# Optimization experiments

Hardware: AMD Instinct MI355X
Metric: run time of the kernel (lower is better)

The kernel has to match this reference:

```python
import jax, jax.numpy as jnp
import numpy as np

N_ENT = 100000   # n_entities
N_REL = 64       # n_relations
E_DIM = 64       # e_dim == r_dim (rel2ent is None)
K = 32           # neighbors per entity
B = 1024         # batch of seed entities
SLOPE = 0.2      # LeakyReLU negative_slope


def _xavier(key, shape, fan_in, fan_out):
    b = (6.0 / (fan_in + fan_out)) ** 0.5
    return jax.random.uniform(key, shape, jnp.float32, -b, b)


def setup_inputs() -> dict:
    key = jax.random.key(0)
    ks = jax.random.split(key, 10)
    E = _xavier(ks[0], (N_ENT, E_DIM), N_ENT, E_DIM)          # entity_embs.weight
    R = _xavier(ks[1], (N_REL, E_DIM), N_REL, E_DIM)          # relation_embs.weight
    att_w1 = _xavier(ks[2], (E_DIM, 2 * E_DIM), 2 * E_DIM, E_DIM)  # attention[0], no bias
    att_w2 = _xavier(ks[3], (E_DIM, E_DIM), E_DIM, E_DIM)          # attention[2], no bias
    att_w3 = _xavier(ks[4], (1, E_DIM), E_DIM, 1)                  # attention[4], no bias
    wx_w = _xavier(ks[5], (E_DIM, E_DIM), E_DIM, E_DIM)            # Wx[0].weight
    wx_b = jnp.zeros((E_DIM,), jnp.float32)                        # Wx[0].bias
    wc_w = _xavier(ks[6], (E_DIM, 2 * E_DIM), 2 * E_DIM, E_DIM)    # W_concat.weight
    wc_b = jnp.zeros((E_DIM,), jnp.float32)                        # W_concat.bias
    entity_idx = jax.random.randint(ks[7], (B,), 0, N_ENT)
    adj_entity = jax.random.randint(ks[8], (N_ENT, K), 0, N_ENT)
    adj_relation = jax.random.randint(ks[9], (N_ENT, K), 0, N_REL)
    return {
        "entity_idx": entity_idx, "adj_entity": adj_entity, "adj_relation": adj_relation,
        "E": E, "R": R, "att_w1": att_w1, "att_w2": att_w2, "att_w3": att_w3,
        "wx_w": wx_w, "wx_b": wx_b, "wc_w": wc_w, "wc_b": wc_b,
    }


def _lookup(W, idx):
    # nn.Embedding(max_norm=1): rows whose L2 norm exceeds 1 are renormalized.
    e = W[idx]
    n = jnp.linalg.norm(e, axis=-1, keepdims=True)
    return e * jnp.where(n > 1.0, 1.0 / (n + 1e-7), 1.0)


def _forward(entity_idx, adj_entity, adj_relation, E, R,
             att_w1, att_w2, att_w3, wx_w, wx_b, wc_w, wc_b):
    leaky = lambda x: jnp.where(x >= 0, x, SLOPE * x)
    # attention MLP on cat([h, r]): split first linear so the broadcast h term
    # is computed once per batch row instead of materializing [B, N, 2e].
    w1h, w1r = att_w1[:, :E_DIM], att_w1[:, E_DIM:]

    def gat(h, r, t):
        # h: [B, e] (broadcast over neighbors), r,t: [B, N, e]
        hid = jax.nn.relu(jnp.einsum('be,fe->bf', h, w1h)[:, None, :]
                          + jnp.einsum('bne,fe->bnf', r, w1r))
        hid = jax.nn.relu(jnp.einsum('bnf,gf->bng', hid, att_w2))
        a = jax.nn.sigmoid(jnp.einsum('bng,og->bno', hid, att_w3)[..., 0])  # [B, N]
        w = jax.nn.softmax(a, axis=-1)
        agg = jnp.einsum('bn,bne->be', w, t)       # softmax-weighted neighbor sum
        return agg @ wx_w.T + wx_b                 # per-head Linear (n_heads=1)

    Bsz = entity_idx.shape[0]
    # hop-1 / hop-2 neighbor index gathers (get_neighbors)
    ent1 = adj_entity[entity_idx]                  # [B, K]
    rel1 = adj_relation[entity_idx]                # [B, K]
    ent2 = adj_entity[ent1].reshape(Bsz, -1)       # [B, K*K]
    rel2 = adj_relation[ent1].reshape(Bsz, -1)     # [B, K*K]

    h = _lookup(E, entity_idx)                     # [B, e]
    t1 = _lookup(E, ent1)                          # [B, K, e]
    t2 = _lookup(E, ent2)                          # [B, K*K, e]
    r1 = _lookup(R, rel1)
    r2 = _lookup(R, rel2)

    # iter 0: seed entity broadcast as head
    v1 = leaky(gat(h, r1, t1))                                      # [B, e]
    emb1 = leaky(jnp.concatenate([h, v1], -1) @ wc_w.T + wc_b)      # aggregate 'concat'
    # iter 1: summed hop-1 neighborhood as head
    hsum = t1.sum(axis=1)                                           # [B, e]
    v2 = leaky(gat(hsum, r2, t2))
    emb2 = leaky(jnp.concatenate([hsum, v2], -1) @ wc_w.T + wc_b)
    # sum_aggregator 'concat': e_u = cat(embs[2], cat(embs[1], embs[0]))
    return jnp.concatenate([emb2, emb1, h], axis=-1)                # [B, 3e]


def reference(entity_idx, adj_entity, adj_relation, E, R,
              att_w1, att_w2, att_w3, wx_w, wx_b, wc_w, wc_b):
    return _forward(entity_idx, adj_entity, adj_relation, E, R,
                    att_w1, att_w2, att_w3, wx_w, wx_b, wc_w, wc_b)
```

## Files before the change

kernel.cpp:

```cpp
#include <hip/hip_runtime.h>

#define SLOPE 0.2f

__device__ __forceinline__ float leaky(float x) { return x >= 0.f ? x : SLOPE * x; }

enum : int {
  OFF_PT   = 0,
  OFF_W2T  = OFF_PT + 4096,
  OFF_A3   = OFF_W2T + 4096,
  OFF_WXT  = OFF_A3 + 64,
  OFF_WXB  = OFF_WXT + 4096,
  OFF_WCT  = OFF_WXB + 64,
  OFF_WCB  = OFF_WCT + 8192,
  OFF_W1HT = OFF_WCB + 64,
  WS_FLOATS = OFF_W1HT + 4096,
  EBF_U32  = 3200000
};

__global__ __launch_bounds__(256) void k1_prep(
    const float* __restrict__ R, const float* __restrict__ w1,
    const float* __restrict__ w2, const float* __restrict__ w3,
    const float* __restrict__ wxw, const float* __restrict__ wxb,
    const float* __restrict__ wcw, const float* __restrict__ wcb,
    const float* __restrict__ E, float* __restrict__ ws) {
  int tid = threadIdx.x;
  if (blockIdx.x >= 8) {
    const float4* E4 = (const float4*)E;
    unsigned long long* Ebf2 =
        (unsigned long long*)((unsigned*)ws + WS_FLOATS);
    int nvec = EBF_U32 / 2;
    int stride = (gridDim.x - 8) * 256;
    for (int i = (blockIdx.x - 8) * 256 + tid; i < nvec; i += stride) {
      float4 f = E4[i];
      unsigned ua = __float_as_uint(f.x); ua += 0x7FFFu + ((ua >> 16) & 1u);
      unsigned ub = __float_as_uint(f.y); ub += 0x7FFFu + ((ub >> 16) & 1u);
      unsigned uc = __float_as_uint(f.z); uc += 0x7FFFu + ((uc >> 16) & 1u);
      unsigned ud = __float_as_uint(f.w); ud += 0x7FFFu + ((ud >> 16) & 1u);
      unsigned lo = (ua >> 16) | (ub & 0xFFFF0000u);
      unsigned hi = (uc >> 16) | (ud & 0xFFFF0000u);
      unsigned long long o = (unsigned long long)lo |
                             ((unsigned long long)hi << 32);
      __builtin_nontemporal_store(o, &Ebf2[i]);
    }
    return;
  }
  __shared__ float Rn[64 * 65];
  int wv = tid >> 6, lane = tid & 63;
  for (int r = wv; r < 64; r += 4) {
    float v = R[r * 64 + lane];
    float ss = v * v;
    #pragma unroll
    for (int m = 1; m < 64; m <<= 1) ss += __shfl_xor(ss, m, 64);
    float n = sqrtf(ss);
    float sc = n > 1.f ? 1.f / (n + 1e-7f) : 1.f;
    Rn[r * 65 + lane] = v * sc;
  }
  __syncthreads();
  int gt = blockIdx.x * 256 + tid;
  for (int i = gt; i < 4096; i += 2048) {
    int f = i >> 6, r = i & 63;
    float acc = 0.f;
    #pragma unroll
    for (int e = 0; e < 64; ++e) acc += Rn[r * 65 + e] * w1[f * 128 + 64 + e];
    ws[OFF_PT + f * 64 + r] = acc;
  }
  for (int i = gt; i < 4096; i += 2048) {
    int f = i >> 6, g = i & 63;
    ws[OFF_W2T + i] = w2[g * 64 + f];
  }
  for (int i = gt; i < 4096; i += 2048) {
    int e = i >> 6, f = i & 63;
    ws[OFF_WXT + i]  = wxw[f * 64 + e];
    ws[OFF_W1HT + i] = w1[f * 128 + e];
  }
  for (int i = gt; i < 8192; i += 2048) {
    int e = i >> 6, f = i & 63;
    ws[OFF_WCT + i] = wcw[f * 128 + e];
  }
  if (gt < 64) {
    ws[OFF_A3 + gt]  = w3[gt];
    ws[OFF_WXB + gt] = wxb[gt];
    ws[OFF_WCB + gt] = wcb[gt];
  }
}

__global__ __launch_bounds__(256) void k_main(
    const int* __restrict__ entity_idx, const int* __restrict__ adj_entity,
    const int* __restrict__ adj_relation, const float* __restrict__ E,
    const float* __restrict__ ws, float* __restrict__ out) {
  __shared__ float s_t1[32 * 64];
  __shared__ float s_partA[4][64], s_partB[4][64];
  __shared__ int   s_ent1[32], s_rel1[32];
  __shared__ unsigned s_ei[1024];
  __shared__ float s_w[1024];
  __shared__ float s_h[64], s_hs[64], s_hq1[64], s_hq2[64];
  __shared__ float s_at1[64], s_at2[64], s_agg1[64], s_agg2[64], s_v1[64], s_v2[64];
  __shared__ float s_L1, s_L2;
  int b = blockIdx.x, tid = threadIdx.x, wv = tid >> 6, lane = tid & 63;
  int idx = entity_idx[b];

  if (tid < 64) s_h[tid] = E[(long)idx * 64 + tid];
  if (tid >= 64 && tid < 96) {
    int i = tid - 64;
    s_ent1[i] = adj_entity[(long)idx * 32 + i];
    s_rel1[i] = adj_relation[(long)idx * 32 + i];
  }
  if (tid == 0) s_L2 = 0.f;
  __syncthreads();

  #pragma unroll
  for (int i = 0; i < 4; ++i) {
    int n = tid + i * 256;
    int j = n >> 5, i2 = n & 31;
    long base = (long)s_ent1[j] * 32 + i2;
    unsigned ei = (unsigned)adj_entity[base];
    unsigned ri = (unsigned)adj_relation[base];
    s_ei[n] = ei | (ri << 24);
  }
  {
    float hs = 0.f;
    #pragma unroll
    for (int k = 0; k < 8; ++k) {
      int n = wv * 8 + k;
      float v = E[(long)s_ent1[n] * 64 + lane];
      s_t1[n * 64 + lane] = v;
      hs += v;
    }
    s_partA[wv][lane] = hs;
  }
  __syncthreads();
  if (tid < 64)
    s_hs[tid] = s_partA[0][tid] + s_partA[1][tid] + s_partA[2][tid] + s_partA[3][tid];
  __syncthreads();

  {
    const float* src = (wv < 2) ? s_h : s_hs;
    int e0 = (wv & 1) * 32;
    float p = 0.f;
    #pragma unroll 8
    for (int e = 0; e < 32; ++e) p += ws[OFF_W1HT + (e0 + e) * 64 + lane] * src[e0 + e];
    s_partB[wv][lane] = p;
  }
  __syncthreads();
  if (tid < 64) s_hq1[tid] = s_partB[0][tid] + s_partB[1][tid];
  else if (tid < 128) { int i = tid - 64; s_hq2[i] = s_partB[2][i] + s_partB[3][i]; }
  __syncthreads();

  {
    int swv = __builtin_amdgcn_readfirstlane(wv);
    const float* W2T = ws + OFF_W2T;
    const float* A3  = ws + OFF_A3;
    const float* PT  = ws + OFF_PT;
    float acc2[16];
    #pragma unroll
    for (int i = 0; i < 16; ++i) acc2[i] = 0.f;
    int g0 = swv * 16;
    #pragma unroll 2
    for (int f = 0; f < 64; ++f) {
      float ptv = PT[f * 64 + lane];
      float h2 = fmaxf(s_hq2[f] + ptv, 0.f);
      const float* w = W2T + f * 64 + g0;
      #pragma unroll
      for (int i = 0; i < 16; ++i) acc2[i] += w[i] * h2;
    }
    float s2 = 0.f;
    #pragma unroll
    for (int i = 0; i < 16; ++i) s2 += A3[g0 + i] * fmaxf(acc2[i], 0.f);
    s_partB[wv][lane] = s2;
  }
  __syncthreads();
  if (tid < 64) {
    float t = s_partB[0][tid] + s_partB[1][tid] + s_partB[2][tid] + s_partB[3][tid];
    float a = 1.f / (1.f + __expf(-t));
    s_at2[tid] = __expf(a);
  }
  __syncthreads();

  {
    float wsum = 0.f;
    #pragma unroll
    for (int i = 0; i < 4; ++i) {
      int n = tid + i * 256;
      float wgt = s_at2[s_ei[n] >> 24];
      s_w[n] = wgt;
      wsum += wgt;
    }
    #pragma unroll
    for (int m = 1; m < 64; m <<= 1) wsum += __shfl_xor(wsum, m, 64);
    if (lane == 0) atomicAdd(&s_L2, wsum);
  }
  __syncthreads();

  {
    const uint4* Ebf = (const uint4*)((const unsigned*)ws + WS_FLOATS);
    int sub8 = lane >> 3, eg8 = lane & 7;
    int rbase = wv * 8 + sub8;
    int swv = __builtin_amdgcn_readfirstlane(wv);
    const float* W2T = ws + OFF_W2T;
    const float* A3  = ws + OFF_A3;
    const float* PT  = ws + OFF_PT;
    int g0 = swv * 16;
    float acc[8], acc1[16];
    #pragma unroll
    for (int k = 0; k < 8; ++k) acc[k] = 0.f;
    #pragma unroll
    for (int i = 0; i < 16; ++i) acc1[i] = 0.f;

    #pragma unroll 1
    for (int t = 0; t < 8; ++t) {
      uint4 v[4];
      float wgt[4];
      #pragma unroll
      for (int j = 0; j < 4; ++j) {
        int n = (t * 4 + j) * 32 + rbase;
        v[j] = Ebf[(long)(s_ei[n] & 0xFFFFFFu) * 8 + eg8];
        wgt[j] = s_w[n];
      }
      #pragma unroll
      for (int ff = 0; ff < 8; ++ff) {
        int f = t * 8 + ff;
        float ptv = PT[f * 64 + lane];
        float h1 = fmaxf(s_hq1[f] + ptv, 0.f);
        const float* w = W2T + f * 64 + g0;
        #pragma unroll
        for (int i = 0; i < 16; ++i) acc1[i] += w[i] * h1;
      }
      #pragma unroll
      for (int j = 0; j < 4; ++j) {
        float w = wgt[j];
        acc[0] += w * __uint_as_float(v[j].x << 16);
        acc[1] += w * __uint_as_float(v[j].x & 0xFFFF0000u);
        acc[2] += w * __uint_as_float(v[j].y << 16);
        acc[3] += w * __uint_as_float(v[j].y & 0xFFFF0000u);
        acc[4] += w * __uint_as_float(v[j].z << 16);
        acc[5] += w * __uint_as_float(v[j].z & 0xFFFF0000u);
        acc[6] += w * __uint_as_float(v[j].w << 16);
        acc[7] += w * __uint_as_float(v[j].w & 0xFFFF0000u);
      }
    }
    float s1 = 0.f;
    #pragma unroll
    for (int i = 0; i < 16; ++i) s1 += A3[g0 + i] * fmaxf(acc1[i], 0.f);
    s_partA[wv][lane] = s1;
    #pragma unroll
    for (int m = 8; m < 64; m <<= 1) {
      #pragma unroll
      for (int k = 0; k < 8; ++k) acc[k] += __shfl_xor(acc[k], m, 64);
    }
    if (sub8 == 0) {
      #pragma unroll
      for (int k = 0; k < 8; ++k) s_partB[wv][eg8 * 8 + k] = acc[k];
    }
  }
  __syncthreads();
  if (tid < 64) {
    float t = s_partA[0][tid] + s_partA[1][tid] + s_partA[2][tid] + s_partA[3][tid];
    float a = 1.f / (1.f + __expf(-t));
    s_at1[tid] = __expf(a);
  } else if (tid < 128) {
    int i = tid - 64;
    float a = s_partB[0][i] + s_partB[1][i] + s_partB[2][i] + s_partB[3][i];
    s_agg2[i] = a / s_L2;
  }
  __syncthreads();

  if (tid < 32) {
    float w = s_at1[s_rel1[tid]];
    #pragma unroll
    for (int m = 1; m < 32; m <<= 1) w += __shfl_xor(w, m, 64);
    if (tid == 0) s_L1 = w;
  }
  {
    float a1 = 0.f;
    #pragma unroll
    for (int k = 0; k < 8; ++k) {
      int n = wv * 8 + k;
      a1 += s_at1[s_rel1[n]] * s_t1[n * 64 + lane];
    }
    s_partA[wv][lane] = a1;
  }
  __syncthreads();
  if (tid < 64) {
    float a = s_partA[0][tid] + s_partA[1][tid] + s_partA[2][tid] + s_partA[3][tid];
    s_agg1[tid] = a / s_L1;
  }
  __syncthreads();

  {
    const float* src = (wv < 2) ? s_agg1 : s_agg2;
    int e0 = (wv & 1) * 32;
    float p = 0.f;
    #pragma unroll 8
    for (int e = 0; e < 32; ++e)
      p += ws[OFF_WXT + (e0 + e) * 64 + lane] * src[e0 + e];
    s_partA[wv][lane] = p;
  }
  __syncthreads();
  if (tid < 64) {
    s_v1[tid] = leaky(ws[OFF_WXB + tid] + s_partA[0][tid] + s_partA[1][tid]);
  } else if (tid < 128) {
    int i = tid - 64;
    s_v2[i] = leaky(ws[OFF_WXB + i] + s_partA[2][i] + s_partA[3][i]);
  }
  __syncthreads();

  {
    const float* src = (wv == 0) ? s_h : (wv == 1) ? s_v1 : (wv == 2) ? s_hs : s_v2;
    int e0 = (wv & 1) * 64;
    float p = 0.f;
    #pragma unroll 8
    for (int e = 0; e < 64; ++e)
      p += ws[OFF_WCT + (e0 + e) * 64 + lane] * src[e];
    s_partB[wv][lane] = p;
  }
  __syncthreads();
  if (tid < 64) {
    float o = ws[OFF_WCB + tid] + s_partB[0][tid] + s_partB[1][tid];
    out[b * 192 + 64 + tid]  = leaky(o);
    out[b * 192 + 128 + tid] = s_h[tid];
  } else if (tid < 128) {
    int i = tid - 64;
    float o = ws[OFF_WCB + i] + s_partB[2][i] + s_partB[3][i];
    out[b * 192 + i] = leaky(o);
  }
}

extern "C" void kernel_launch(void* const* d_in, const int* in_sizes, int n_in,
                              void* d_out, int out_size, void* d_ws, size_t ws_size,
                              hipStream_t stream) {
  const int* entity_idx   = (const int*)d_in[0];
  const int* adj_entity   = (const int*)d_in[1];
  const int* adj_relation = (const int*)d_in[2];
  const float* E          = (const float*)d_in[3];
  const float* R          = (const float*)d_in[4];
  const float* att_w1     = (const float*)d_in[5];
  const float* att_w2     = (const float*)d_in[6];
  const float* att_w3     = (const float*)d_in[7];
  const float* wx_w       = (const float*)d_in[8];
  const float* wx_b       = (const float*)d_in[9];
  const float* wc_w       = (const float*)d_in[10];
  const float* wc_b       = (const float*)d_in[11];
  float* out              = (float*)d_out;
  float* ws               = (float*)d_ws;

  hipLaunchKernelGGL(k1_prep, dim3(1608), dim3(256), 0, stream,
                     R, att_w1, att_w2, att_w3, wx_w, wx_b, wc_w, wc_b, E, ws);
  hipLaunchKernelGGL(k_main, dim3(1024), dim3(256), 0, stream,
                     entity_idx, adj_entity, adj_relation, E, ws, out);
}
```

Baseline: 149.5 us.

## Double k_main block to 512 threads and split per-block work across eight waves

Raises the main kernel from 4 to 8 wavefronts per block. Every stage (hop-2 gather, attention MLP slices, reductions, final linears) is repartitioned so each wave does half as much work, with partial sums reduced over 8 slots. The aim is more latency hiding for the random bf16 gathers and shorter per-wave serial chains. The cost is more partial-sum reduction work, and each block keeps its extra barriers.

```diff
diff --git a/kernel.cpp b/kernel.cpp
--- a/kernel.cpp
+++ b/kernel.cpp
@@ -84,12 +84,12 @@
   }
 }
 
-__global__ __launch_bounds__(256) void k_main(
+__global__ __launch_bounds__(512, 8) void k_main(
     const int* __restrict__ entity_idx, const int* __restrict__ adj_entity,
     const int* __restrict__ adj_relation, const float* __restrict__ E,
     const float* __restrict__ ws, float* __restrict__ out) {
   __shared__ float s_t1[32 * 64];
-  __shared__ float s_partA[4][64], s_partB[4][64];
+  __shared__ float s_partA[8][64], s_partB[8][64];
   __shared__ int   s_ent1[32], s_rel1[32];
   __shared__ unsigned s_ei[1024];
   __shared__ float s_w[1024];
@@ -109,8 +109,8 @@
   __syncthreads();
 
   #pragma unroll
-  for (int i = 0; i < 4; ++i) {
-    int n = tid + i * 256;
+  for (int i = 0; i < 2; ++i) {
+    int n = tid + i * 512;
     int j = n >> 5, i2 = n & 31;
     long base = (long)s_ent1[j] * 32 + i2;
     unsigned ei = (unsigned)adj_entity[base];
@@ -120,8 +120,8 @@
   {
     float hs = 0.f;
     #pragma unroll
-    for (int k = 0; k < 8; ++k) {
-      int n = wv * 8 + k;
+    for (int k = 0; k < 4; ++k) {
+      int n = wv * 4 + k;
       float v = E[(long)s_ent1[n] * 64 + lane];
       s_t1[n * 64 + lane] = v;
       hs += v;
@@ -129,21 +129,29 @@
     s_partA[wv][lane] = hs;
   }
   __syncthreads();
-  if (tid < 64)
-    s_hs[tid] = s_partA[0][tid] + s_partA[1][tid] + s_partA[2][tid] + s_partA[3][tid];
-  __syncthreads();
-
-  {
-    const float* src = (wv < 2) ? s_h : s_hs;
-    int e0 = (wv & 1) * 32;
+  if (tid < 64) {
+    float hs = 0.f;
+    #pragma unroll
+    for (int w = 0; w < 8; ++w) hs += s_partA[w][tid];
+    s_hs[tid] = hs;
+  }
+  __syncthreads();
+
+  {
+    const float* src = (wv < 4) ? s_h : s_hs;
+    int e0 = (wv & 3) * 16;
     float p = 0.f;
     #pragma unroll 8
-    for (int e = 0; e < 32; ++e) p += ws[OFF_W1HT + (e0 + e) * 64 + lane] * src[e0 + e];
+    for (int e = 0; e < 16; ++e) p += ws[OFF_W1HT + (e0 + e) * 64 + lane] * src[e0 + e];
     s_partB[wv][lane] = p;
   }
   __syncthreads();
-  if (tid < 64) s_hq1[tid] = s_partB[0][tid] + s_partB[1][tid];
-  else if (tid < 128) { int i = tid - 64; s_hq2[i] = s_partB[2][i] + s_partB[3][i]; }
+  if (tid < 64) {
+    s_hq1[tid] = s_partB[0][tid] + s_partB[1][tid] + s_partB[2][tid] + s_partB[3][tid];
+  } else if (tid < 128) {
+    int i = tid - 64;
+    s_hq2[i] = s_partB[4][i] + s_partB[5][i] + s_partB[6][i] + s_partB[7][i];
+  }
   __syncthreads();
 
   {
@@ -151,26 +159,28 @@
     const float* W2T = ws + OFF_W2T;
     const float* A3  = ws + OFF_A3;
     const float* PT  = ws + OFF_PT;
-    float acc2[16];
-    #pragma unroll
-    for (int i = 0; i < 16; ++i) acc2[i] = 0.f;
-    int g0 = swv * 16;
+    float acc2[8];
+    #pragma unroll
+    for (int i = 0; i < 8; ++i) acc2[i] = 0.f;
+    int g0 = swv * 8;
     #pragma unroll 2
     for (int f = 0; f < 64; ++f) {
       float ptv = PT[f * 64 + lane];
       float h2 = fmaxf(s_hq2[f] + ptv, 0.f);
       const float* w = W2T + f * 64 + g0;
       #pragma unroll
-      for (int i = 0; i < 16; ++i) acc2[i] += w[i] * h2;
+      for (int i = 0; i < 8; ++i) acc2[i] += w[i] * h2;
     }
     float s2 = 0.f;
     #pragma unroll
-    for (int i = 0; i < 16; ++i) s2 += A3[g0 + i] * fmaxf(acc2[i], 0.f);
+    for (int i = 0; i < 8; ++i) s2 += A3[g0 + i] * fmaxf(acc2[i], 0.f);
     s_partB[wv][lane] = s2;
   }
   __syncthreads();
   if (tid < 64) {
-    float t = s_partB[0][tid] + s_partB[1][tid] + s_partB[2][tid] + s_partB[3][tid];
+    float t = 0.f;
+    #pragma unroll
+    for (int w = 0; w < 8; ++w) t += s_partB[w][tid];
     float a = 1.f / (1.f + __expf(-t));
     s_at2[tid] = __expf(a);
   }
@@ -179,8 +189,8 @@
   {
     float wsum = 0.f;
     #pragma unroll
-    for (int i = 0; i < 4; ++i) {
-      int n = tid + i * 256;
+    for (int i = 0; i < 2; ++i) {
+      int n = tid + i * 512;
       float wgt = s_at2[s_ei[n] >> 24];
       s_w[n] = wgt;
       wsum += wgt;
@@ -199,31 +209,31 @@
     const float* W2T = ws + OFF_W2T;
     const float* A3  = ws + OFF_A3;
     const float* PT  = ws + OFF_PT;
-    int g0 = swv * 16;
-    float acc[8], acc1[16];
+    int g0 = swv * 8;
+    float acc[8], acc1[8];
     #pragma unroll
     for (int k = 0; k < 8; ++k) acc[k] = 0.f;
     #pragma unroll
-    for (int i = 0; i < 16; ++i) acc1[i] = 0.f;
+    for (int i = 0; i < 8; ++i) acc1[i] = 0.f;
 
     #pragma unroll 1
-    for (int t = 0; t < 8; ++t) {
+    for (int t = 0; t < 4; ++t) {
       uint4 v[4];
       float wgt[4];
       #pragma unroll
       for (int j = 0; j < 4; ++j) {
-        int n = (t * 4 + j) * 32 + rbase;
+        int n = (t * 4 + j) * 64 + rbase;
         v[j] = Ebf[(long)(s_ei[n] & 0xFFFFFFu) * 8 + eg8];
         wgt[j] = s_w[n];
       }
       #pragma unroll
-      for (int ff = 0; ff < 8; ++ff) {
-        int f = t * 8 + ff;
+      for (int ff = 0; ff < 16; ++ff) {
+        int f = t * 16 + ff;
         float ptv = PT[f * 64 + lane];
         float h1 = fmaxf(s_hq1[f] + ptv, 0.f);
         const float* w = W2T + f * 64 + g0;
         #pragma unroll
-        for (int i = 0; i < 16; ++i) acc1[i] += w[i] * h1;
+        for (int i = 0; i < 8; ++i) acc1[i] += w[i] * h1;
       }
       #pragma unroll
       for (int j = 0; j < 4; ++j) {
@@ -240,7 +250,7 @@
     }
     float s1 = 0.f;
     #pragma unroll
-    for (int i = 0; i < 16; ++i) s1 += A3[g0 + i] * fmaxf(acc1[i], 0.f);
+    for (int i = 0; i < 8; ++i) s1 += A3[g0 + i] * fmaxf(acc1[i], 0.f);
     s_partA[wv][lane] = s1;
     #pragma unroll
     for (int m = 8; m < 64; m <<= 1) {
@@ -254,12 +264,16 @@
   }
   __syncthreads();
   if (tid < 64) {
-    float t = s_partA[0][tid] + s_partA[1][tid] + s_partA[2][tid] + s_partA[3][tid];
+    float t = 0.f;
+    #pragma unroll
+    for (int w = 0; w < 8; ++w) t += s_partA[w][tid];
     float a = 1.f / (1.f + __expf(-t));
     s_at1[tid] = __expf(a);
   } else if (tid < 128) {
     int i = tid - 64;
-    float a = s_partB[0][i] + s_partB[1][i] + s_partB[2][i] + s_partB[3][i];
+    float a = 0.f;
+    #pragma unroll
+    for (int w = 0; w < 8; ++w) a += s_partB[w][i];
     s_agg2[i] = a / s_L2;
   }
   __syncthreads();
@@ -273,54 +287,65 @@
   {
     float a1 = 0.f;
     #pragma unroll
-    for (int k = 0; k < 8; ++k) {
-      int n = wv * 8 + k;
+    for (int k = 0; k < 4; ++k) {
+      int n = wv * 4 + k;
       a1 += s_at1[s_rel1[n]] * s_t1[n * 64 + lane];
     }
     s_partA[wv][lane] = a1;
   }
   __syncthreads();
   if (tid < 64) {
-    float a = s_partA[0][tid] + s_partA[1][tid] + s_partA[2][tid] + s_partA[3][tid];
+    float a = 0.f;
+    #pragma unroll
+    for (int w = 0; w < 8; ++w) a += s_partA[w][tid];
     s_agg1[tid] = a / s_L1;
   }
   __syncthreads();
 
   {
-    const float* src = (wv < 2) ? s_agg1 : s_agg2;
-    int e0 = (wv & 1) * 32;
+    const float* src = (wv < 4) ? s_agg1 : s_agg2;
+    int e0 = (wv & 3) * 16;
     float p = 0.f;
     #pragma unroll 8
-    for (int e = 0; e < 32; ++e)
+    for (int e = 0; e < 16; ++e)
       p += ws[OFF_WXT + (e0 + e) * 64 + lane] * src[e0 + e];
     s_partA[wv][lane] = p;
   }
   __syncthreads();
   if (tid < 64) {
-    s_v1[tid] = leaky(ws[OFF_WXB + tid] + s_partA[0][tid] + s_partA[1][tid]);
+    s_v1[tid] = leaky(ws[OFF_WXB + tid] + s_partA[0][tid] + s_partA[1][tid] +
+                      s_partA[2][tid] + s_partA[3][tid]);
   } else if (tid < 128) {
     int i = tid - 64;
-    s_v2[i] = leaky(ws[OFF_WXB + i] + s_partA[2][i] + s_partA[3][i]);
-  }
-  __syncthreads();
-
-  {
-    const float* src = (wv == 0) ? s_h : (wv == 1) ? s_v1 : (wv == 2) ? s_hs : s_v2;
-    int e0 = (wv & 1) * 64;
+    s_v2[i] = leaky(ws[OFF_WXB + i] + s_partA[4][i] + s_partA[5][i] +
+                    s_partA[6][i] + s_partA[7][i]);
+  }
+  __syncthreads();
+
+  {
+    int half = (wv >> 2);
+    int e0 = (wv & 3) * 32;
+    const float* lo = half ? s_hs : s_h;
+    const float* hi = half ? s_v2 : s_v1;
     float p = 0.f;
     #pragma unroll 8
-    for (int e = 0; e < 64; ++e)
-      p += ws[OFF_WCT + (e0 + e) * 64 + lane] * src[e];
+    for (int j = 0; j < 32; ++j) {
+      int e = e0 + j;
+      float val = (e < 64) ? lo[e] : hi[e - 64];
+      p += ws[OFF_WCT + e * 64 + lane] * val;
+    }
     s_partB[wv][lane] = p;
   }
   __syncthreads();
   if (tid < 64) {
-    float o = ws[OFF_WCB + tid] + s_partB[0][tid] + s_partB[1][tid];
+    float o = ws[OFF_WCB + tid] + s_partB[0][tid] + s_partB[1][tid] +
+              s_partB[2][tid] + s_partB[3][tid];
     out[b * 192 + 64 + tid]  = leaky(o);
     out[b * 192 + 128 + tid] = s_h[tid];
   } else if (tid < 128) {
     int i = tid - 64;
-    float o = ws[OFF_WCB + i] + s_partB[2][i] + s_partB[3][i];
+    float o = ws[OFF_WCB + i] + s_partB[4][i] + s_partB[5][i] +
+              s_partB[6][i] + s_partB[7][i];
     out[b * 192 + i] = leaky(o);
   }
 }
@@ -345,6 +370,6 @@
 
   hipLaunchKernelGGL(k1_prep, dim3(1608), dim3(256), 0, stream,
                      R, att_w1, att_w2, att_w3, wx_w, wx_b, wc_w, wc_b, E, ws);
-  hipLaunchKernelGGL(k_main, dim3(1024), dim3(256), 0, stream,
+  hipLaunchKernelGGL(k_main, dim3(1024), dim3(512), 0, stream,
                      entity_idx, adj_entity, adj_relation, E, ws, out);
 }
```

New measurement: 178.9 us. +19.7%, slower.

## Overlap bf16 embedding conversion with main compute via in-kernel flag

Applied to the files above, without the earlier changes.

Moves the fp32-to-bf16 entity table conversion out of the prep kernel into the first blocks of the main kernel. The remaining blocks run the hop-1 and relation-weight work concurrently and spin on a global atomic counter only before they need the bf16 table. This is meant to hide the conversion pass behind the main work and drop a kernel boundary. The risk is a deadlock if the waiting blocks occupy the GPU before all converter blocks get scheduled, though the low block indices are normally dispatched first. It also drops the nontemporal stores.

```diff
diff --git a/kernel.cpp b/kernel.cpp
--- a/kernel.cpp
+++ b/kernel.cpp
@@ -14,23 +14,70 @@
   OFF_WCB  = OFF_WCT + 8192,
   OFF_W1HT = OFF_WCB + 64,
   WS_FLOATS = OFF_W1HT + 4096,
-  EBF_U32  = 3200000
+  EBF_U32  = 3200000,
+  OFF_FLAG = WS_FLOATS + EBF_U32
 };
+
+#define NCONV 1600
 
 __global__ __launch_bounds__(256) void k1_prep(
     const float* __restrict__ R, const float* __restrict__ w1,
     const float* __restrict__ w2, const float* __restrict__ w3,
     const float* __restrict__ wxw, const float* __restrict__ wxb,
     const float* __restrict__ wcw, const float* __restrict__ wcb,
-    const float* __restrict__ E, float* __restrict__ ws) {
-  int tid = threadIdx.x;
-  if (blockIdx.x >= 8) {
+    float* __restrict__ ws) {
+  __shared__ float Rn[64 * 65];
+  int tid = threadIdx.x, wv = tid >> 6, lane = tid & 63;
+  if (blockIdx.x == 0 && tid == 0) ((unsigned*)ws)[OFF_FLAG] = 0u;
+  for (int r = wv; r < 64; r += 4) {
+    float v = R[r * 64 + lane];
+    float ss = v * v;
+    #pragma unroll
+    for (int m = 1; m < 64; m <<= 1) ss += __shfl_xor(ss, m, 64);
+    float n = sqrtf(ss);
+    float sc = n > 1.f ? 1.f / (n + 1e-7f) : 1.f;
+    Rn[r * 65 + lane] = v * sc;
+  }
+  __syncthreads();
+  int gt = blockIdx.x * 256 + tid;
+  for (int i = gt; i < 4096; i += 2048) {
+    int f = i >> 6, r = i & 63;
+    float acc = 0.f;
+    #pragma unroll
+    for (int e = 0; e < 64; ++e) acc += Rn[r * 65 + e] * w1[f * 128 + 64 + e];
+    ws[OFF_PT + f * 64 + r] = acc;
+  }
+  for (int i = gt; i < 4096; i += 2048) {
+    int f = i >> 6, g = i & 63;
+    ws[OFF_W2T + i] = w2[g * 64 + f];
+  }
+  for (int i = gt; i < 4096; i += 2048) {
+    int e = i >> 6, f = i & 63;
+    ws[OFF_WXT + i]  = wxw[f * 64 + e];
+    ws[OFF_W1HT + i] = w1[f * 128 + e];
+  }
+  for (int i = gt; i < 8192; i += 2048) {
+    int e = i >> 6, f = i & 63;
+    ws[OFF_WCT + i] = wcw[f * 128 + e];
+  }
+  if (gt < 64) {
+    ws[OFF_A3 + gt]  = w3[gt];
+    ws[OFF_WXB + gt] = wxb[gt];
+    ws[OFF_WCB + gt] = wcb[gt];
+  }
+}
+
+__global__ __launch_bounds__(256) void k_all(
+    const int* __restrict__ entity_idx, const int* __restrict__ adj_entity,
+    const int* __restrict__ adj_relation, const float* __restrict__ E,
+    float* __restrict__ ws, float* __restrict__ out) {
+  unsigned* flagp = (unsigned*)ws + OFF_FLAG;
+  if (blockIdx.x < NCONV) {
     const float4* E4 = (const float4*)E;
-    unsigned long long* Ebf2 =
-        (unsigned long long*)((unsigned*)ws + WS_FLOATS);
+    unsigned long long* Ebf2 = (unsigned long long*)((unsigned*)ws + WS_FLOATS);
     int nvec = EBF_U32 / 2;
-    int stride = (gridDim.x - 8) * 256;
-    for (int i = (blockIdx.x - 8) * 256 + tid; i < nvec; i += stride) {
+    int stride = NCONV * 256;
+    for (int i = blockIdx.x * 256 + threadIdx.x; i < nvec; i += stride) {
       float4 f = E4[i];
       unsigned ua = __float_as_uint(f.x); ua += 0x7FFFu + ((ua >> 16) & 1u);
       unsigned ub = __float_as_uint(f.y); ub += 0x7FFFu + ((ub >> 16) & 1u);
@@ -38,56 +85,15 @@
       unsigned ud = __float_as_uint(f.w); ud += 0x7FFFu + ((ud >> 16) & 1u);
       unsigned lo = (ua >> 16) | (ub & 0xFFFF0000u);
       unsigned hi = (uc >> 16) | (ud & 0xFFFF0000u);
-      unsigned long long o = (unsigned long long)lo |
-                             ((unsigned long long)hi << 32);
-      __builtin_nontemporal_store(o, &Ebf2[i]);
-    }
+      Ebf2[i] = (unsigned long long)lo | ((unsigned long long)hi << 32);
+    }
+    __threadfence();
+    __syncthreads();
+    if (threadIdx.x == 0)
+      __hip_atomic_fetch_add(flagp, 1u, __ATOMIC_RELEASE, __HIP_MEMORY_SCOPE_AGENT);
     return;
   }
-  __shared__ float Rn[64 * 65];
-  int wv = tid >> 6, lane = tid & 63;
-  for (int r = wv; r < 64; r += 4) {
-    float v = R[r * 64 + lane];
-    float ss = v * v;
-    #pragma unroll
-    for (int m = 1; m < 64; m <<= 1) ss += __shfl_xor(ss, m, 64);
-    float n = sqrtf(ss);
-    float sc = n > 1.f ? 1.f / (n + 1e-7f) : 1.f;
-    Rn[r * 65 + lane] = v * sc;
-  }
-  __syncthreads();
-  int gt = blockIdx.x * 256 + tid;
-  for (int i = gt; i < 4096; i += 2048) {
-    int f = i >> 6, r = i & 63;
-    float acc = 0.f;
-    #pragma unroll
-    for (int e = 0; e < 64; ++e) acc += Rn[r * 65 + e] * w1[f * 128 + 64 + e];
-    ws[OFF_PT + f * 64 + r] = acc;
-  }
-  for (int i = gt; i < 4096; i += 2048) {
-    int f = i >> 6, g = i & 63;
-    ws[OFF_W2T + i] = w2[g * 64 + f];
-  }
-  for (int i = gt; i < 4096; i += 2048) {
-    int e = i >> 6, f = i & 63;
-    ws[OFF_WXT + i]  = wxw[f * 64 + e];
-    ws[OFF_W1HT + i] = w1[f * 128 + e];
-  }
-  for (int i = gt; i < 8192; i += 2048) {
-    int e = i >> 6, f = i & 63;
-    ws[OFF_WCT + i] = wcw[f * 128 + e];
-  }
-  if (gt < 64) {
-    ws[OFF_A3 + gt]  = w3[gt];
-    ws[OFF_WXB + gt] = wxb[gt];
-    ws[OFF_WCB + gt] = wcb[gt];
-  }
-}
-
-__global__ __launch_bounds__(256) void k_main(
-    const int* __restrict__ entity_idx, const int* __restrict__ adj_entity,
-    const int* __restrict__ adj_relation, const float* __restrict__ E,
-    const float* __restrict__ ws, float* __restrict__ out) {
+
   __shared__ float s_t1[32 * 64];
   __shared__ float s_partA[4][64], s_partB[4][64];
   __shared__ int   s_ent1[32], s_rel1[32];
@@ -96,7 +102,7 @@
   __shared__ float s_h[64], s_hs[64], s_hq1[64], s_hq2[64];
   __shared__ float s_at1[64], s_at2[64], s_agg1[64], s_agg2[64], s_v1[64], s_v2[64];
   __shared__ float s_L1, s_L2;
-  int b = blockIdx.x, tid = threadIdx.x, wv = tid >> 6, lane = tid & 63;
+  int b = blockIdx.x - NCONV, tid = threadIdx.x, wv = tid >> 6, lane = tid & 63;
   int idx = entity_idx[b];
 
   if (tid < 64) s_h[tid] = E[(long)idx * 64 + tid];
@@ -188,6 +194,13 @@
     #pragma unroll
     for (int m = 1; m < 64; m <<= 1) wsum += __shfl_xor(wsum, m, 64);
     if (lane == 0) atomicAdd(&s_L2, wsum);
+  }
+  __syncthreads();
+
+  if (tid == 0) {
+    while (__hip_atomic_load(flagp, __ATOMIC_ACQUIRE, __HIP_MEMORY_SCOPE_AGENT)
+           < (unsigned)NCONV)
+      __builtin_amdgcn_s_sleep(8);
   }
   __syncthreads();
 
@@ -343,8 +356,8 @@
   float* out              = (float*)d_out;
   float* ws               = (float*)d_ws;
 
-  hipLaunchKernelGGL(k1_prep, dim3(1608), dim3(256), 0, stream,
-                     R, att_w1, att_w2, att_w3, wx_w, wx_b, wc_w, wc_b, E, ws);
-  hipLaunchKernelGGL(k_main, dim3(1024), dim3(256), 0, stream,
+  hipLaunchKernelGGL(k1_prep, dim3(8), dim3(256), 0, stream,
+                     R, att_w1, att_w2, att_w3, wx_w, wx_b, wc_w, wc_b, ws);
+  hipLaunchKernelGGL(k_all, dim3(NCONV + 1024), dim3(256), 0, stream,
                      entity_idx, adj_entity, adj_relation, E, ws, out);
 }
```

Measured after the change: 327.2 us. 119% more time.
